# Kernel optimization log

Measured on AMD Instinct MI355X. Metric: run time of the kernel, lower is better.

Reference implementation:

```python
import jax, jax.numpy as jnp
import numpy as np

LX, LY = 32, 32
FILTER, STRIDE = 4, 1
DEL = FILTER - STRIDE  # 3


def setup_inputs() -> dict:
    key = jax.random.key(0)
    k1, k2, k3 = jax.random.split(key, 3)
    x = jax.random.normal(k1, (128, 256, LX, LY), dtype=jnp.float32)
    W = jax.random.normal(k2, (512, 256, FILTER, FILTER), dtype=jnp.float32) * 0.02
    b = jax.random.normal(k3, (512,), dtype=jnp.float32) * 0.02
    return {"x": x, "W": W, "b": b}


def _pbc_pad(x):
    # Faithful equivalent of tensordot(x, getPbcTensor(...), dims=2):
    # eye(Lx*Ly, (Lx+d)*(Ly+d)) copies by FLAT index into the larger buffer,
    # then the corner entries T[i,j,i+Lx,j+Ly]=1 (i,j<d) ADD x[:, :, :d, :d].
    B, C = x.shape[0], x.shape[1]
    n_in = LX * LY
    n_out = (LX + DEL) * (LY + DEL)
    flat = jnp.zeros((B, C, n_out), dtype=x.dtype)
    flat = flat.at[..., :n_in].set(x.reshape(B, C, n_in))
    pad = flat.reshape(B, C, LX + DEL, LY + DEL)
    pad = pad.at[:, :, LX:, LY:].add(x[:, :, :DEL, :DEL])
    return pad


def reference(x, W, b):
    pad = _pbc_pad(x)  # (B, C, Lx+3, Ly+3) = (B, C, 35, 35)
    y = jax.lax.conv_general_dilated(
        pad, W, window_strides=(STRIDE, STRIDE), padding='VALID',
        dimension_numbers=('NCHW', 'OIHW', 'NCHW'))
    return y + b[None, :, None, None]  # (B, 512, 32, 32)
```

## Files before the change

kernel.cpp:

```cpp
#include <hip/hip_runtime.h>


#define BM 128
#define BN 128

typedef __attribute__((ext_vector_type(8))) short short8;
typedef __attribute__((ext_vector_type(4))) float f32x4;

struct __attribute__((packed)) u16x4 { unsigned short a, b, c, d; };

__device__ __forceinline__ unsigned short f2bf(float f) {
    union { float f; unsigned u; } v; v.f = f;
    unsigned r = v.u + 0x7FFF + ((v.u >> 16) & 1);
    return (unsigned short)(r >> 16);
}

__device__ __forceinline__ void async_b128(const void* g, void* l) {
    __builtin_amdgcn_global_load_lds(
        (const __attribute__((address_space(1))) void*)g,
        (__attribute__((address_space(3))) void*)l, 16, 0, 0);
}

__global__ __launch_bounds__(256) void build_pad_vec(const float* __restrict__ x,
                                                     unsigned short* __restrict__ xp) {
    const int bc = blockIdx.x;
    const int t  = threadIdx.x;
    if (t >= 154) return;
    const float* xb = x + (long)bc * 1024;
    union { unsigned short h[8]; short8 v; } u;
    if (t < 128) {
        const float4 f0 = *(const float4*)(xb + t * 8);
        const float4 f1 = *(const float4*)(xb + t * 8 + 4);
        u.h[0] = f2bf(f0.x); u.h[1] = f2bf(f0.y); u.h[2] = f2bf(f0.z); u.h[3] = f2bf(f0.w);
        u.h[4] = f2bf(f1.x); u.h[5] = f2bf(f1.y); u.h[6] = f2bf(f1.z); u.h[7] = f2bf(f1.w);
    } else {
        #pragma unroll
        for (int e = 0; e < 8; ++e) {
            const int v = t * 8 + e;
            const int p = (v * 7490) >> 18;
            const int q = v - p * 35;
            float val = 0.0f;
            if (p >= 32 && q >= 32) val = xb[((p - 32) << 5) + (q - 32)];
            u.h[e] = f2bf(val);
        }
    }
    *(short8*)(xp + (long)bc * 1232 + t * 8) = u.v;
}

__global__ __launch_bounds__(256) void build_pad_s(const float* __restrict__ x,
                                                   unsigned short* __restrict__ xp) {
    const int v = blockIdx.x * 256 + threadIdx.x;
    const int bc = blockIdx.y;
    if (v >= 1225) return;
    const int p = (v * 7490) >> 18;
    const int q = v - p * 35;
    const float* xb = x + (long)bc * 1024;
    float val = (v < 1024) ? xb[v] : 0.0f;
    if (p >= 32 && q >= 32) val += xb[((p - 32) << 5) + (q - 32)];
    xp[(long)bc * 1225 + v] = f2bf(val);
}

__global__ __launch_bounds__(256) void cvt_w(const float* __restrict__ W,
                                             unsigned short* __restrict__ Wb) {
    const int i = (blockIdx.x * 256 + threadIdx.x) * 8;
    const float4 f0 = *(const float4*)(W + i);
    const float4 f1 = *(const float4*)(W + i + 4);
    union { unsigned short h[8]; short8 v; } u;
    u.h[0] = f2bf(f0.x); u.h[1] = f2bf(f0.y); u.h[2] = f2bf(f0.z); u.h[3] = f2bf(f0.w);
    u.h[4] = f2bf(f1.x); u.h[5] = f2bf(f1.y); u.h[6] = f2bf(f1.z); u.h[7] = f2bf(f1.w);
    *(short8*)(Wb + i) = u.v;
}

__global__ __launch_bounds__(256) void convpbc_mfma3(
    const unsigned short* __restrict__ xpad,
    const unsigned short* __restrict__ Wb,
    const float* __restrict__ bias,
    float* __restrict__ y,
    const int cstride)
{
    __shared__ __attribute__((aligned(16))) unsigned short Blds[2 * BN * 32];

    const int tid = threadIdx.x;
    const int bid = blockIdx.x;
    const int nt = bid & 3;
    const int mt = bid >> 2;
    const int batch = mt >> 3;
    const int s0 = (mt & 7) * BM;
    const int i0 = (mt & 7) * 4;

    const int lane = tid & 63;
    const int w    = tid >> 6;
    const int wm   = (w >> 1) * 64;
    const int wn   = (w & 1) * 64;
    const int lr   = lane & 15;
    const int quad = lane >> 4;

    const int fi0 = (quad & 1) * 2;
    const unsigned short* ab = xpad + (long)(batch * 256 + (quad >> 1)) * cstride;
    int aoff[4];
    #pragma unroll
    for (int mi = 0; mi < 4; ++mi) {
        const int i_mi = i0 + (wm >> 5) + (mi >> 1) + fi0;
        const int j_mi = (mi & 1) * 16 + lr;
        aoff[mi] = i_mi * 35 + j_mi;
    }
    const int cs2 = 2 * cstride;
    const int cs4 = 4 * cstride;

    const int brow0 = w * 32 + (lane >> 2);
    const int brow1 = brow0 + 16;
    const int bseg  = lane & 3;
    const unsigned short* bg0 =
        Wb + (long)(nt * BN + brow0) * 4096 + (bseg ^ ((brow0 >> 1) & 3)) * 8;
    const unsigned short* bg1 =
        Wb + (long)(nt * BN + brow1) * 4096 + (bseg ^ ((brow1 >> 1) & 3)) * 8;
    unsigned short* const bl0_0 = &Blds[(w * 32) * 32];
    unsigned short* const bl1_0 = bl0_0 + 512;
    unsigned short* const bl0_1 = bl0_0 + 4096;
    unsigned short* const bl1_1 = bl0_0 + 4608;

    int bfaddr[4];
    #pragma unroll
    for (int ni = 0; ni < 4; ++ni) {
        const int row = wn + ni * 16 + lr;
        bfaddr[ni] = row * 32 + (quad ^ ((row >> 1) & 3)) * 8;
    }

    f32x4 acc[4][4] = {};
    short8 afA[4], afB[4];

    #define LOAD_A(dst, base)                                                    \
        _Pragma("unroll")                                                        \
        for (int mi = 0; mi < 4; ++mi) {                                         \
            union { unsigned short h[8]; short8 f; } u_;                         \
            *(u16x4*)&u_.h[0] = *(const u16x4*)((base) + aoff[mi]);              \
            *(u16x4*)&u_.h[4] = *(const u16x4*)((base) + aoff[mi] + 35);         \
            dst[mi] = u_.f;                                                      \
        }

    async_b128(bg0, bl0_0);
    async_b128(bg1, bl1_0);
    LOAD_A(afA, ab)

    const unsigned short* abs_ = ab;

    for (int k0 = 0; k0 < 4096; k0 += 64) {
        __syncthreads();

        async_b128(bg0 + k0 + 32, bl0_1);
        async_b128(bg1 + k0 + 32, bl1_1);
        LOAD_A(afB, abs_ + cs2)

        {
            short8 bf[4];
            #pragma unroll
            for (int ni = 0; ni < 4; ++ni)
                bf[ni] = *(const short8*)&Blds[bfaddr[ni]];
            #pragma unroll
            for (int mi = 0; mi < 4; ++mi)
                #pragma unroll
                for (int ni = 0; ni < 4; ++ni)
                    acc[mi][ni] = __builtin_amdgcn_mfma_f32_16x16x32_bf16(
                        afA[mi], bf[ni], acc[mi][ni], 0, 0, 0);
        }

        __syncthreads();

        if (k0 + 64 < 4096) {
            async_b128(bg0 + k0 + 64, bl0_0);
            async_b128(bg1 + k0 + 64, bl1_0);
            LOAD_A(afA, abs_ + cs4)
        }

        {
            short8 bf[4];
            #pragma unroll
            for (int ni = 0; ni < 4; ++ni)
                bf[ni] = *(const short8*)&Blds[4096 + bfaddr[ni]];
            #pragma unroll
            for (int mi = 0; mi < 4; ++mi)
                #pragma unroll
                for (int ni = 0; ni < 4; ++ni)
                    acc[mi][ni] = __builtin_amdgcn_mfma_f32_16x16x32_bf16(
                        afB[mi], bf[ni], acc[mi][ni], 0, 0, 0);
        }

        abs_ += cs4;
    }
    #undef LOAD_A

    #pragma unroll
    for (int ni = 0; ni < 4; ++ni) {
        const int ngl = nt * BN + wn + ni * 16 + lr;
        const float bv = bias[ngl];
        float* ybase = y + (((long)(batch * 512 + ngl)) << 10) + s0;
        #pragma unroll
        for (int mi = 0; mi < 4; ++mi) {
            const int mbase = wm + mi * 16 + quad * 4;
            #pragma unroll
            for (int r = 0; r < 4; ++r)
                ybase[mbase + r] = acc[mi][ni][r] + bv;
        }
    }
}

#define LDA 40
#define LDB 40
__global__ __launch_bounds__(256) void convpbc_mfma(
    const float* __restrict__ x, const float* __restrict__ W,
    const float* __restrict__ bias, float* __restrict__ y)
{
    __shared__ __attribute__((aligned(16))) unsigned short Alds[BM * LDA];
    __shared__ __attribute__((aligned(16))) unsigned short BldsL[BN * LDB];
    const int tid = threadIdx.x, bid = blockIdx.x;
    const int nt = bid & 3, mt = bid >> 2, batch = mt >> 3;
    const int s0 = (mt & 7) * BM;
    const int lane = tid & 63, w = tid >> 6;
    const int wm = (w >> 1) * 64, wn = (w & 1) * 64;
    const int lr = lane & 15, quad = lane >> 4;
    const int sm = tid >> 1, half = tid & 1;
    const int s = s0 + sm, i0 = s >> 5, j0 = s & 31;
    const float* wrow = W + (long)(nt * BN + sm) * 4096;
    f32x4 acc[4][4] = {};
    for (int k0 = 0; k0 < 4096; k0 += 32) {
        {
            const int c = (k0 >> 4) + half;
            const float* xp = x + (((long)(batch * 256 + c)) << 10);
            __attribute__((aligned(16))) unsigned short tmp[16];
            #pragma unroll
            for (int t = 0; t < 16; ++t) {
                const int p = i0 + (t >> 2), q = j0 + (t & 3);
                const int v = p * 35 + q;
                const bool corner = (p >= 32) & (q >= 32);
                const bool valid = corner | (v < 1024);
                int idx = corner ? (((p - 32) << 5) + (q - 32)) : v;
                idx = valid ? idx : 0;
                float fv = xp[idx];
                fv = valid ? fv : 0.0f;
                tmp[t] = f2bf(fv);
            }
            short8* dst = (short8*)&Alds[sm * LDA + half * 16];
            dst[0] = *(const short8*)&tmp[0];
            dst[1] = *(const short8*)&tmp[8];
        }
        {
            const float4* wv = (const float4*)(wrow + k0 + half * 16);
            __attribute__((aligned(16))) unsigned short tmp[16];
            #pragma unroll
            for (int t4 = 0; t4 < 4; ++t4) {
                const float4 f = wv[t4];
                tmp[t4 * 4 + 0] = f2bf(f.x); tmp[t4 * 4 + 1] = f2bf(f.y);
                tmp[t4 * 4 + 2] = f2bf(f.z); tmp[t4 * 4 + 3] = f2bf(f.w);
            }
            short8* dst = (short8*)&BldsL[sm * LDB + half * 16];
            dst[0] = *(const short8*)&tmp[0];
            dst[1] = *(const short8*)&tmp[8];
        }
        __syncthreads();
        short8 af[4], bf[4];
        #pragma unroll
        for (int mi = 0; mi < 4; ++mi)
            af[mi] = *(const short8*)&Alds[(wm + mi * 16 + lr) * LDA + quad * 8];
        #pragma unroll
        for (int ni = 0; ni < 4; ++ni)
            bf[ni] = *(const short8*)&BldsL[(wn + ni * 16 + lr) * LDB + quad * 8];
        #pragma unroll
        for (int mi = 0; mi < 4; ++mi)
            #pragma unroll
            for (int ni = 0; ni < 4; ++ni)
                acc[mi][ni] = __builtin_amdgcn_mfma_f32_16x16x32_bf16(
                    af[mi], bf[ni], acc[mi][ni], 0, 0, 0);
        __syncthreads();
    }
    #pragma unroll
    for (int ni = 0; ni < 4; ++ni) {
        const int ngl = nt * BN + wn + ni * 16 + lr;
        const float bv = bias[ngl];
        float* ybase = y + (((long)(batch * 512 + ngl)) << 10) + s0;
        #pragma unroll
        for (int mi = 0; mi < 4; ++mi) {
            const int mbase = wm + mi * 16 + quad * 4;
            #pragma unroll
            for (int r = 0; r < 4; ++r)
                ybase[mbase + r] = acc[mi][ni][r] + bv;
        }
    }
}

extern "C" void kernel_launch(void* const* d_in, const int* in_sizes, int n_in,
                              void* d_out, int out_size, void* d_ws, size_t ws_size,
                              hipStream_t stream) {
    const float* x    = (const float*)d_in[0];
    const float* W    = (const float*)d_in[1];
    const float* bias = (const float*)d_in[2];
    float* y          = (float*)d_out;

    const size_t W_ELEMS = 512L * 4096;
    const size_t XPAD_P  = 128L * 256 * 1232;
    const size_t XPAD_S  = 128L * 256 * 1225;
    const size_t NEED_P  = (XPAD_P + W_ELEMS) * 2;
    const size_t NEED_S  = (XPAD_S + W_ELEMS) * 2;

    if (ws_size >= NEED_P) {
        unsigned short* xpad = (unsigned short*)d_ws;
        unsigned short* Wb   = xpad + XPAD_P;
        hipLaunchKernelGGL(build_pad_vec, dim3(128 * 256), dim3(256), 0, stream, x, xpad);
        hipLaunchKernelGGL(cvt_w, dim3(1024), dim3(256), 0, stream, W, Wb);
        hipLaunchKernelGGL(convpbc_mfma3, dim3(4096), dim3(256), 0, stream,
                           xpad, Wb, bias, y, 1232);
    } else if (ws_size >= NEED_S) {
        unsigned short* xpad = (unsigned short*)d_ws;
        unsigned short* Wb   = xpad + XPAD_S;
        hipLaunchKernelGGL(build_pad_s, dim3(5, 128 * 256), dim3(256), 0, stream, x, xpad);
        hipLaunchKernelGGL(cvt_w, dim3(1024), dim3(256), 0, stream, W, Wb);
        hipLaunchKernelGGL(convpbc_mfma3, dim3(4096), dim3(256), 0, stream,
                           xpad, Wb, bias, y, 1225);
    } else {
        hipLaunchKernelGGL(convpbc_mfma, dim3(4096), dim3(256), 0, stream, x, W, bias, y);
    }
}
```

Measured before the change: 1.402 ms.

## Deepen conv GEMM pipeline to four LDS stages with vmcnt waits and XCD remap

Replaces the double-buffered main loop with a 4-stage ring of LDS buffers and register A-fragments. It uses explicit s_waitcnt vmcnt and raw s_barrier so loads stay in flight across several compute steps, and raises priority around the MFMA blocks. It also remaps block IDs so neighbouring tiles land on the same XCD for L2 reuse. It sets launch_bounds to 3 waves per EU and packs the pad-build kernel densely so fewer threads sit idle. Costs are higher LDS and register use, and the hand-counted vmcnt values must stay correct.

```diff
diff --git a/kernel.cpp b/kernel.cpp
--- a/kernel.cpp
+++ b/kernel.cpp
@@ -21,11 +21,12 @@
         (__attribute__((address_space(3))) void*)l, 16, 0, 0);
 }
 
-__global__ __launch_bounds__(256) void build_pad_vec(const float* __restrict__ x,
-                                                     unsigned short* __restrict__ xp) {
-    const int bc = blockIdx.x;
-    const int t  = threadIdx.x;
-    if (t >= 154) return;
+__global__ __launch_bounds__(256) void build_pad_vec2(const float* __restrict__ x,
+                                                      unsigned short* __restrict__ xp) {
+    const int idx = blockIdx.x * 256 + threadIdx.x;
+    const int bc  = idx / 154;
+    const int t   = idx - bc * 154;
+    if (bc >= 32768) return;
     const float* xb = x + (long)bc * 1024;
     union { unsigned short h[8]; short8 v; } u;
     if (t < 128) {
@@ -71,17 +72,17 @@
     *(short8*)(Wb + i) = u.v;
 }
 
-__global__ __launch_bounds__(256) void convpbc_mfma3(
+__global__ __launch_bounds__(256, 3) void convpbc_mfma4(
     const unsigned short* __restrict__ xpad,
     const unsigned short* __restrict__ Wb,
     const float* __restrict__ bias,
     float* __restrict__ y,
     const int cstride)
 {
-    __shared__ __attribute__((aligned(16))) unsigned short Blds[2 * BN * 32];
+    __shared__ __attribute__((aligned(16))) unsigned short Blds[4 * 4096];
 
     const int tid = threadIdx.x;
-    const int bid = blockIdx.x;
+    const int bid = (blockIdx.x & 7) * 512 + (blockIdx.x >> 3);
     const int nt = bid & 3;
     const int mt = bid >> 2;
     const int batch = mt >> 3;
@@ -104,8 +105,7 @@
         const int j_mi = (mi & 1) * 16 + lr;
         aoff[mi] = i_mi * 35 + j_mi;
     }
-    const int cs2 = 2 * cstride;
-    const int cs4 = 4 * cstride;
+    const int csStep = 2 * cstride;
 
     const int brow0 = w * 32 + (lane >> 2);
     const int brow1 = brow0 + 16;
@@ -114,10 +114,8 @@
         Wb + (long)(nt * BN + brow0) * 4096 + (bseg ^ ((brow0 >> 1) & 3)) * 8;
     const unsigned short* bg1 =
         Wb + (long)(nt * BN + brow1) * 4096 + (bseg ^ ((brow1 >> 1) & 3)) * 8;
-    unsigned short* const bl0_0 = &Blds[(w * 32) * 32];
-    unsigned short* const bl1_0 = bl0_0 + 512;
-    unsigned short* const bl0_1 = bl0_0 + 4096;
-    unsigned short* const bl1_1 = bl0_0 + 4608;
+    unsigned short* const blA = &Blds[(w * 32) * 32];
+    unsigned short* const blB = blA + 512;
 
     int bfaddr[4];
     #pragma unroll
@@ -127,67 +125,68 @@
     }
 
     f32x4 acc[4][4] = {};
-    short8 afA[4], afB[4];
-
-    #define LOAD_A(dst, base)                                                    \
-        _Pragma("unroll")                                                        \
-        for (int mi = 0; mi < 4; ++mi) {                                         \
-            union { unsigned short h[8]; short8 f; } u_;                         \
-            *(u16x4*)&u_.h[0] = *(const u16x4*)((base) + aoff[mi]);              \
-            *(u16x4*)&u_.h[4] = *(const u16x4*)((base) + aoff[mi] + 35);         \
-            dst[mi] = u_.f;                                                      \
-        }
-
-    async_b128(bg0, bl0_0);
-    async_b128(bg1, bl1_0);
-    LOAD_A(afA, ab)
-
-    const unsigned short* abs_ = ab;
-
-    for (int k0 = 0; k0 < 4096; k0 += 64) {
-        __syncthreads();
-
-        async_b128(bg0 + k0 + 32, bl0_1);
-        async_b128(bg1 + k0 + 32, bl1_1);
-        LOAD_A(afB, abs_ + cs2)
-
-        {
-            short8 bf[4];
-            #pragma unroll
-            for (int ni = 0; ni < 4; ++ni)
-                bf[ni] = *(const short8*)&Blds[bfaddr[ni]];
-            #pragma unroll
-            for (int mi = 0; mi < 4; ++mi)
-                #pragma unroll
-                for (int ni = 0; ni < 4; ++ni)
-                    acc[mi][ni] = __builtin_amdgcn_mfma_f32_16x16x32_bf16(
-                        afA[mi], bf[ni], acc[mi][ni], 0, 0, 0);
-        }
-
-        __syncthreads();
-
-        if (k0 + 64 < 4096) {
-            async_b128(bg0 + k0 + 64, bl0_0);
-            async_b128(bg1 + k0 + 64, bl1_0);
-            LOAD_A(afA, abs_ + cs4)
-        }
-
-        {
-            short8 bf[4];
-            #pragma unroll
-            for (int ni = 0; ni < 4; ++ni)
-                bf[ni] = *(const short8*)&Blds[4096 + bfaddr[ni]];
-            #pragma unroll
-            for (int mi = 0; mi < 4; ++mi)
-                #pragma unroll
-                for (int ni = 0; ni < 4; ++ni)
-                    acc[mi][ni] = __builtin_amdgcn_mfma_f32_16x16x32_bf16(
-                        afB[mi], bf[ni], acc[mi][ni], 0, 0, 0);
-        }
-
-        abs_ += cs4;
-    }
-    #undef LOAD_A
+    short8 af0[4], af1[4], af2[4], af3[4];
+
+    const unsigned short* bg0i = bg0;
+    const unsigned short* bg1i = bg1;
+    const unsigned short* abi  = ab;
+
+    #define ISSUE_B(BUF, OFF)                                                  \
+        async_b128(bg0i + (OFF) * 32, blA + (BUF) * 4096);                     \
+        async_b128(bg1i + (OFF) * 32, blB + (BUF) * 4096);
+    #define ISSUE_A(SET, OFF)                                                  \
+        {                                                                      \
+            const unsigned short* ap_ = abi + (OFF) * csStep;                  \
+            _Pragma("unroll")                                                  \
+            for (int mi = 0; mi < 4; ++mi) {                                   \
+                union { unsigned short h[8]; short8 f; } u_;                   \
+                *(u16x4*)&u_.h[0] = *(const u16x4*)(ap_ + aoff[mi]);           \
+                *(u16x4*)&u_.h[4] = *(const u16x4*)(ap_ + aoff[mi] + 35);      \
+                SET[mi] = u_.f;                                                \
+            }                                                                  \
+        }
+    #define BARRIER_WAIT(N)                                                    \
+        asm volatile("s_waitcnt vmcnt(" #N ")" ::: "memory");                  \
+        __builtin_amdgcn_s_barrier();                                          \
+        __builtin_amdgcn_sched_barrier(0);
+    #define COMPUTE_STEP(SET, BUF)                                             \
+        {                                                                      \
+            short8 bf[4];                                                      \
+            _Pragma("unroll")                                                  \
+            for (int ni = 0; ni < 4; ++ni)                                     \
+                bf[ni] = *(const short8*)&Blds[(BUF) * 4096 + bfaddr[ni]];     \
+            __builtin_amdgcn_s_setprio(1);                                     \
+            _Pragma("unroll")                                                  \
+            for (int mi = 0; mi < 4; ++mi)                                     \
+                _Pragma("unroll")                                              \
+                for (int ni = 0; ni < 4; ++ni)                                 \
+                    acc[mi][ni] = __builtin_amdgcn_mfma_f32_16x16x32_bf16(     \
+                        SET[mi], bf[ni], acc[mi][ni], 0, 0, 0);                \
+            __builtin_amdgcn_s_setprio(0);                                     \
+        }
+
+    ISSUE_B(0, 0)
+    ISSUE_B(1, 1)
+    ISSUE_A(af0, 0)
+    ISSUE_B(2, 2)
+    ISSUE_A(af1, 1)
+
+    for (int kb = 0; kb < 31; ++kb) {
+        BARRIER_WAIT(10) ISSUE_B(3, 3) ISSUE_A(af2, 2) COMPUTE_STEP(af0, 0)
+        BARRIER_WAIT(10) ISSUE_B(0, 4) ISSUE_A(af3, 3) COMPUTE_STEP(af1, 1)
+        BARRIER_WAIT(10) ISSUE_B(1, 5) ISSUE_A(af0, 4) COMPUTE_STEP(af2, 2)
+        BARRIER_WAIT(10) ISSUE_B(2, 6) ISSUE_A(af1, 5) COMPUTE_STEP(af3, 3)
+        bg0i += 128; bg1i += 128; abi += 4 * csStep;
+    }
+    BARRIER_WAIT(10) ISSUE_B(3, 3) ISSUE_A(af2, 2) COMPUTE_STEP(af0, 0)
+    BARRIER_WAIT(10) ISSUE_A(af3, 3)               COMPUTE_STEP(af1, 1)
+    BARRIER_WAIT(8)                                COMPUTE_STEP(af2, 2)
+    BARRIER_WAIT(0)                                COMPUTE_STEP(af3, 3)
+
+    #undef ISSUE_B
+    #undef ISSUE_A
+    #undef BARRIER_WAIT
+    #undef COMPUTE_STEP
 
     #pragma unroll
     for (int ni = 0; ni < 4; ++ni) {
@@ -304,16 +303,16 @@
     if (ws_size >= NEED_P) {
         unsigned short* xpad = (unsigned short*)d_ws;
         unsigned short* Wb   = xpad + XPAD_P;
-        hipLaunchKernelGGL(build_pad_vec, dim3(128 * 256), dim3(256), 0, stream, x, xpad);
+        hipLaunchKernelGGL(build_pad_vec2, dim3(19712), dim3(256), 0, stream, x, xpad);
         hipLaunchKernelGGL(cvt_w, dim3(1024), dim3(256), 0, stream, W, Wb);
-        hipLaunchKernelGGL(convpbc_mfma3, dim3(4096), dim3(256), 0, stream,
+        hipLaunchKernelGGL(convpbc_mfma4, dim3(4096), dim3(256), 0, stream,
                            xpad, Wb, bias, y, 1232);
     } else if (ws_size >= NEED_S) {
         unsigned short* xpad = (unsigned short*)d_ws;
         unsigned short* Wb   = xpad + XPAD_S;
         hipLaunchKernelGGL(build_pad_s, dim3(5, 128 * 256), dim3(256), 0, stream, x, xpad);
         hipLaunchKernelGGL(cvt_w, dim3(1024), dim3(256), 0, stream, W, Wb);
-        hipLaunchKernelGGL(convpbc_mfma3, dim3(4096), dim3(256), 0, stream,
+        hipLaunchKernelGGL(convpbc_mfma4, dim3(4096), dim3(256), 0, stream,
                            xpad, Wb, bias, y, 1225);
     } else {
         hipLaunchKernelGGL(convpbc_mfma, dim3(4096), dim3(256), 0, stream, x, W, bias, y);
```

After: 1.738 ms. 23.9% more time.
